# Kernel tuning notes

Measured on AMD Instinct MI355X. Metric: run time of the kernel, lower is better.

The kernel has to match this reference:

```python
import jax, jax.numpy as jnp
import numpy as np

DT = 0.02        # time step
DT_SKIP = DT * 20
ITERS = 49       # BDF2 iterations hardcoded in forward()
P = 64           # tronc (reduced dim)
NG_U = 8000      # HR sample count, u-equation
NG_V = 8000      # HR sample count, v-equation
B = 32           # batch of trajectories


def setup_inputs() -> dict:
    key = jax.random.key(0)
    k0, k1, k2, k3, k4 = jax.random.split(key, 5)
    state = jax.random.normal(k0, (B, P), dtype=jnp.float32)
    Ap = jax.random.normal(k1, (P, P), dtype=jnp.float32) * 0.05
    W_all_u = jax.random.normal(k2, (4 * NG_U, P), dtype=jnp.float32) * 0.02
    W_all_v = jax.random.normal(k3, (4 * NG_V, P), dtype=jnp.float32) * 0.02
    P_proj = jax.random.normal(k4, (P, NG_U + NG_V), dtype=jnp.float32) * 0.02
    return {"state": state, "Ap": Ap, "W_all_u": W_all_u,
            "W_all_v": W_all_v, "P_proj": P_proj}


def _rhs(a, W_all_u, W_all_v, P_proj):
    # a: (B, p) -> (B, p). Batched hyper-reduced quadratic RHS.
    zu = a @ W_all_u.T                       # (B, 4*Ng_u)
    uu, vu, dxu, dyu = jnp.split(zu, 4, axis=1)
    fu = uu * dxu + vu * dyu                 # (B, Ng_u)
    zv = a @ W_all_v.T                       # (B, 4*Ng_v)
    uv, vv, dxv, dyv = jnp.split(zv, 4, axis=1)
    fv = uv * dxv + vv * dyv                 # (B, Ng_v)
    concat = jnp.concatenate([fu, fv], axis=1)  # (B, Ng_u+Ng_v)
    return -(concat @ P_proj.T)              # (B, p)


def reference(state, Ap, W_all_u, W_all_v, P_proj):
    dt = jnp.float32(DT)
    a0 = state[:, :P]                        # state_rom (B, p)
    eye = jnp.eye(P, dtype=state.dtype)
    mat_1st = eye - dt * Ap[:P, :P]          # I - dt*A
    mat_2nd = 3.0 * eye - 2.0 * dt * Ap[:P, :P]

    # first step: implicit Euler
    f0 = _rhs(a0, W_all_u, W_all_v, P_proj)
    r0 = a0 + dt * f0
    a1 = jnp.linalg.solve(mat_1st, r0.T).T   # == lu_solve(LU_1st, ...)

    # BDF2 recurrence
    def step(carry, _):
        a_prev, f_prev, a_new = carry
        f_new = _rhs(a_new, W_all_u, W_all_v, P_proj)
        r = 4.0 * a_new - a_prev + 4.0 * dt * f_new - 2.0 * dt * f_prev
        a_next = jnp.linalg.solve(mat_2nd, r.T).T
        return (a_new, f_new, a_next), None

    (_, _, out_new), _ = jax.lax.scan(step, (a0, f0, a1), None, length=ITERS)
    return (out_new - a0) / jnp.float32(DT_SKIP)
```

## Files before the change

### kernel.cpp

```cpp
#include <hip/hip_runtime.h>

#define DTC 0.02f
#define INV_DT_SKIP 2.5f
#define NBLK 32
#define NSTEP 50

typedef __attribute__((ext_vector_type(8))) __bf16 bf16x8;
typedef __attribute__((ext_vector_type(4))) float f32x4;
typedef __attribute__((ext_vector_type(8))) unsigned short us8;
typedef unsigned long long u64t;

__device__ inline unsigned short f2bf(float x) {
    unsigned u = __float_as_uint(x);
    unsigned r = u + 0x7FFF + ((u >> 16) & 1u);
    return (unsigned short)(r >> 16);
}
__device__ inline float bf2f(unsigned short h) {
    return __uint_as_float(((unsigned)h) << 16);
}
__device__ inline unsigned short f2bf_force(float x, unsigned b) {
    unsigned u = __float_as_uint(x);
    unsigned short c1 = (unsigned short)(((u >> 16) & ~1u) | b);
    unsigned short c0 = (unsigned short)(c1 - 2);
    unsigned short c2 = (unsigned short)(c1 + 2);
    float d0 = fabsf(x - bf2f(c0));
    float d1 = fabsf(x - bf2f(c1));
    float d2 = fabsf(x - bf2f(c2));
    unsigned short h = c1; float d = d1;
    if (d0 < d) { h = c0; d = d0; }
    if (d2 < d) { h = c2; }
    return h;
}
__device__ inline void gstore32(unsigned* p, unsigned v) {
    __hip_atomic_store(p, v, __ATOMIC_RELAXED, __HIP_MEMORY_SCOPE_AGENT);
}
__device__ inline u64t gload64(const u64t* p) {
    return __hip_atomic_load(p, __ATOMIC_RELAXED, __HIP_MEMORY_SCOPE_AGENT);
}
#define PINV(x) asm volatile("" : "+v"(x))

__global__ __launch_bounds__(256) void kinv(const float* __restrict__ Ap,
                                            float* __restrict__ inv1,
                                            float* __restrict__ inv2,
                                            uint4* __restrict__ pz) {
    const int t = threadIdx.x;
    {
        const int gt = blockIdx.x * 256 + t;
        for (int i = gt; i < 16384; i += 512) pz[i] = (uint4){0u, 0u, 0u, 0u};
    }
    const float coef  = (blockIdx.x == 0) ? DTC : (2.0f * DTC / 3.0f);
    const float scale = (blockIdx.x == 0) ? 1.0f : (1.0f / 3.0f);
    float* outp = (blockIdx.x == 0) ? inv1 : inv2;

    __shared__ float ET[64 * 68];
    __shared__ float XA[64 * 68];
    __shared__ float XB[64 * 68];

    for (int idx = t; idx < 4096; idx += 256) {
        int r = idx >> 6, c = idx & 63;
        float e = coef * Ap[idx];
        ET[c * 68 + r] = e;
        XA[r * 68 + c] = ((r == c) ? 1.0f : 0.0f) + e;
    }
    __syncthreads();

    const int rr = (t >> 4) << 2;
    const int cc = (t & 15) << 2;
    float* bufs[2] = {XA, XB};
    for (int it = 0; it < 3; it++) {
        const float* Xin = bufs[it & 1];
        float* Xout = bufs[(it + 1) & 1];
        float acc[4][4];
        #pragma unroll
        for (int i = 0; i < 4; i++)
            #pragma unroll
            for (int j = 0; j < 4; j++)
                acc[i][j] = ((rr + i) == (cc + j)) ? 1.0f : 0.0f;
        for (int k = 0; k < 64; k++) {
            float4 e4 = *(const float4*)&ET[k * 68 + rr];
            float4 x4 = *(const float4*)&Xin[k * 68 + cc];
            float ev[4] = {e4.x, e4.y, e4.z, e4.w};
            float xv[4] = {x4.x, x4.y, x4.z, x4.w};
            #pragma unroll
            for (int i = 0; i < 4; i++)
                #pragma unroll
                for (int j = 0; j < 4; j++)
                    acc[i][j] += ev[i] * xv[j];
        }
        __syncthreads();
        #pragma unroll
        for (int i = 0; i < 4; i++)
            #pragma unroll
            for (int j = 0; j < 4; j++)
                Xout[(rr + i) * 68 + cc + j] = acc[i][j];
        __syncthreads();
    }
    const float* Xf = bufs[1];
    for (int idx = t; idx < 4096; idx += 256) {
        int r = idx >> 6, c = idx & 63;
        outp[idx] = scale * Xf[r * 68 + c];
    }
}

__global__ __launch_bounds__(512, 2)
void kmain(const float* __restrict__ state,
           const float* __restrict__ Wu,
           const float* __restrict__ Wv,
           const float* __restrict__ Pp,
           const float* __restrict__ inv1,
           const float* __restrict__ inv2,
           unsigned* __restrict__ pbuf,
           float* __restrict__ out) {
    const int t = threadIdx.x;
    const int l = t & 63;
    const int w = t >> 6;
    const int blk = blockIdx.x;
    const int gw = blk * 8 + w;
    const bool active = (gw < 250);

    __shared__ float Ab[3][2176];
    __shared__ float fb[8][16][36];
    __shared__ float red2[2][8][1056];
    __shared__ float rbuf[32 * 68];

    for (int i = t; i < 2048; i += 512) Ab[0][(i >> 6) * 68 + (i & 63)] = state[i];
    if (!active) {
        for (int i = l; i < 1056; i += 64) { red2[0][w][i] = 0.f; red2[1][w][i] = 0.f; }
    }

    const int nr = l & 15;
    const int c0 = (l >> 4) << 3;
    const int cA = gw * 2;
    const float* W = (cA < 250) ? Wu : Wv;
    const int glA = ((cA < 250) ? cA : cA - 250) * 32;

    bf16x8 wf[2][2][4][2], pf[2][4], sfw[2];
    if (active) {
        #pragma unroll
        for (int ch = 0; ch < 2; ch++)
            #pragma unroll
            for (int th = 0; th < 2; th++)
                #pragma unroll
                for (int rb = 0; rb < 4; rb++)
                    #pragma unroll
                    for (int kt = 0; kt < 2; kt++) {
                        const float* s = W + (size_t)(rb * 8000 + glA + ch * 32 + th * 16 + nr) * 64
                                           + kt * 32 + c0;
                        us8 o;
                        #pragma unroll
                        for (int j = 0; j < 8; j++) o[j] = f2bf(s[j]);
                        wf[ch][th][rb][kt] = __builtin_bit_cast(bf16x8, o);
                    }
        #pragma unroll
        for (int ch = 0; ch < 2; ch++)
            #pragma unroll
            for (int pt = 0; pt < 4; pt++) {
                const float* s = Pp + (size_t)(pt * 16 + nr) * 16000 + (cA + ch) * 32 + c0;
                us8 o;
                #pragma unroll
                for (int j = 0; j < 8; j++) o[j] = f2bf(s[j]);
                pf[ch][pt] = __builtin_bit_cast(bf16x8, o);
            }
    }
    {
        const int ptS = w & 3;
        #pragma unroll
        for (int kt = 0; kt < 2; kt++) {
            int p = ptS * 16 + nr;
            const float* s = inv2 + (size_t)p * 64 + kt * 32 + c0;
            us8 o;
            #pragma unroll
            for (int j = 0; j < 8; j++) {
                float v = s[j] - ((p == kt * 32 + c0 + j) ? (1.0f / 3.0f) : 0.0f);
                o[j] = f2bf(v);
            }
            sfw[kt] = __builtin_bit_cast(bf16x8, o);
        }
    }
    #pragma unroll
    for (int ch = 0; ch < 2; ch++) {
        #pragma unroll
        for (int th = 0; th < 2; th++)
            #pragma unroll
            for (int rb = 0; rb < 4; rb++)
                #pragma unroll
                for (int kt = 0; kt < 2; kt++) PINV(wf[ch][th][rb][kt]);
        #pragma unroll
        for (int pt = 0; pt < 4; pt++) PINV(pf[ch][pt]);
    }
    PINV(sfw[0]); PINV(sfw[1]);
    __syncthreads();

    int ia_prev = 2, ia_cur = 0, ia_next = 1;
    float fprev[4];

    for (int k = 0; k < NSTEP; k++) {
        const int par = k & 1;
        const unsigned tag2 = (unsigned)(k + 1) & 3u;
        unsigned* pslot = pbuf + (size_t)par * (NBLK * 1024) + blk * 1024;

        if (active) {
            const int col = l & 15, q4 = l >> 4;
            #pragma unroll
            for (int mt = 0; mt < 2; mt++) {
                bf16x8 ahi[2], alo[2];
                {
                    const float* ac = Ab[ia_cur];
                    #pragma unroll
                    for (int kt = 0; kt < 2; kt++) {
                        us8 hv, lv;
                        #pragma unroll
                        for (int j = 0; j < 8; j++) {
                            float x = ac[(mt * 16 + nr) * 68 + kt * 32 + c0 + j];
                            unsigned short h = f2bf(x);
                            hv[j] = h;
                            lv[j] = f2bf(x - bf2f(h));
                        }
                        ahi[kt] = __builtin_bit_cast(bf16x8, hv);
                        alo[kt] = __builtin_bit_cast(bf16x8, lv);
                    }
                }
                f32x4 racc[4] = {{0.f,0.f,0.f,0.f},{0.f,0.f,0.f,0.f},
                                 {0.f,0.f,0.f,0.f},{0.f,0.f,0.f,0.f}};
                #pragma unroll
                for (int ch = 0; ch < 2; ch++) {
                    #pragma unroll
                    for (int th = 0; th < 2; th++) {
                        f32x4 z[4];
                        #pragma unroll
                        for (int rb = 0; rb < 4; rb++) {
                            f32x4 acc = {0.f, 0.f, 0.f, 0.f};
                            #pragma unroll
                            for (int kt = 0; kt < 2; kt++) {
                                acc = __builtin_amdgcn_mfma_f32_16x16x32_bf16(ahi[kt], wf[ch][th][rb][kt], acc, 0, 0, 0);
                                acc = __builtin_amdgcn_mfma_f32_16x16x32_bf16(alo[kt], wf[ch][th][rb][kt], acc, 0, 0, 0);
                            }
                            z[rb] = acc;
                        }
                        #pragma unroll
                        for (int r = 0; r < 4; r++) {
                            float f = z[0][r] * z[2][r] + z[1][r] * z[3][r];
                            fb[w][q4 * 4 + r][th * 16 + col] = f;
                        }
                    }
                    bf16x8 ff;
                    {
                        us8 fv8;
                        #pragma unroll
                        for (int j = 0; j < 8; j++) fv8[j] = f2bf(fb[w][nr][c0 + j]);
                        ff = __builtin_bit_cast(bf16x8, fv8);
                    }
                    #pragma unroll
                    for (int pt = 0; pt < 4; pt++)
                        racc[pt] = __builtin_amdgcn_mfma_f32_16x16x32_bf16(ff, pf[ch][pt], racc[pt], 0, 0, 0);
                }
                #pragma unroll
                for (int pt = 0; pt < 4; pt++)
                    #pragma unroll
                    for (int r = 0; r < 4; r++)
                        red2[mt][w][q4 * 264 + r * 64 + pt * 16 + col] = racc[pt][r];
            }
        }
        __syncthreads();

        {
            const int q4e = t >> 7;
            const int rem = (2 * t) & 255;
            const int addr = q4e * 264 + rem;
            #pragma unroll
            for (int mt = 0; mt < 2; mt++) {
                float s0 = 0.f, s1 = 0.f;
                #pragma unroll
                for (int w8 = 0; w8 < 8; w8++) {
                    float2 p = *(const float2*)&red2[mt][w8][addr];
                    s0 += p.x;
                    s1 += p.y;
                }
                unsigned v = (unsigned)f2bf_force(s0, tag2 & 1u)
                           | ((unsigned)f2bf_force(s1, tag2 >> 1) << 16);
                gstore32(&pslot[mt * 512 + t], v);
            }
        }

        float rb_[4];
        const int bB = (4 * t) >> 6, p0B = (4 * t) & 63;
        {
            #pragma unroll
            for (int jj = 0; jj < 4; jj++) {
                int row = bB * 68 + p0B + jj;
                float av = Ab[ia_cur][row];
                rb_[jj] = (k == 0) ? av
                                   : (4.f * av - Ab[ia_prev][row] - 2.f * DTC * fprev[jj]);
            }
        }

        float fv[4];
        {
            const u64t* pb = (const u64t*)(pbuf + (size_t)par * (NBLK * 1024));
            const unsigned tagrep = (tag2 & 1u) | ((tag2 >> 1) << 16);
            float s0 = 0.f, s1 = 0.f, s2 = 0.f, s3 = 0.f;
            unsigned need = 0xFFFFFFFFu;
            for (;;) {
                u64t buf[NBLK];
                #pragma unroll
                for (int s = 0; s < NBLK; s++)
                    buf[s] = gload64(pb + (size_t)s * 512 + t);
                #pragma unroll
                for (int s = 0; s < NBLK; s++) {
                    unsigned lo = (unsigned)buf[s], hi = (unsigned)(buf[s] >> 32);
                    unsigned bad = ((lo ^ tagrep) | (hi ^ tagrep)) & 0x00010001u;
                    if (((need >> s) & 1u) && bad == 0u) {
                        s0 += __uint_as_float(lo << 16);
                        s1 += __uint_as_float(lo & 0xffff0000u);
                        s2 += __uint_as_float(hi << 16);
                        s3 += __uint_as_float(hi & 0xffff0000u);
                        need &= ~(1u << s);
                    }
                }
                if (!__any(need != 0u)) break;
                __builtin_amdgcn_s_sleep(2);
            }
            asm volatile("" ::: "memory");
            fv[0] = -s0; fv[1] = -s1; fv[2] = -s2; fv[3] = -s3;
        }

        {
            const float cf = (k == 0) ? DTC : 4.f * DTC;
            #pragma unroll
            for (int jj = 0; jj < 4; jj++) {
                float f = fv[jj];
                rbuf[bB * 68 + p0B + jj] = rb_[jj] + cf * f;
                fprev[jj] = f;
            }
        }
        __syncthreads();

        {
            const int mtS = w >> 2, ptS = w & 3;
            const int col = l & 15, q4 = l >> 4;
            bf16x8 S0, S1;
            float cb;
            if (k == 0) {
                #pragma unroll
                for (int kt = 0; kt < 2; kt++) {
                    int p = ptS * 16 + nr;
                    const float* s = inv1 + (size_t)p * 64 + kt * 32 + c0;
                    us8 o;
                    #pragma unroll
                    for (int j = 0; j < 8; j++) {
                        float v = s[j] - ((p == kt * 32 + c0 + j) ? 1.0f : 0.0f);
                        o[j] = f2bf(v);
                    }
                    if (kt == 0) S0 = __builtin_bit_cast(bf16x8, o);
                    else         S1 = __builtin_bit_cast(bf16x8, o);
                }
                cb = 1.0f;
            } else {
                S0 = sfw[0]; S1 = sfw[1];
                cb = 1.0f / 3.0f;
            }
            bf16x8 rhi[2], rlo[2];
            #pragma unroll
            for (int kt = 0; kt < 2; kt++) {
                us8 hv, lv;
                #pragma unroll
                for (int j = 0; j < 8; j++) {
                    float x = rbuf[(mtS * 16 + nr) * 68 + kt * 32 + c0 + j];
                    unsigned short h = f2bf(x);
                    hv[j] = h;
                    lv[j] = f2bf(x - bf2f(h));
                }
                rhi[kt] = __builtin_bit_cast(bf16x8, hv);
                rlo[kt] = __builtin_bit_cast(bf16x8, lv);
            }
            f32x4 acc;
            #pragma unroll
            for (int r = 0; r < 4; r++)
                acc[r] = rbuf[(mtS * 16 + q4 * 4 + r) * 68 + ptS * 16 + col] * cb;
            acc = __builtin_amdgcn_mfma_f32_16x16x32_bf16(rhi[0], S0, acc, 0, 0, 0);
            acc = __builtin_amdgcn_mfma_f32_16x16x32_bf16(rlo[0], S0, acc, 0, 0, 0);
            acc = __builtin_amdgcn_mfma_f32_16x16x32_bf16(rhi[1], S1, acc, 0, 0, 0);
            acc = __builtin_amdgcn_mfma_f32_16x16x32_bf16(rlo[1], S1, acc, 0, 0, 0);
            #pragma unroll
            for (int r = 0; r < 4; r++)
                Ab[ia_next][(mtS * 16 + q4 * 4 + r) * 68 + ptS * 16 + col] = acc[r];
        }
        __syncthreads();

        if (k == NSTEP - 1 && blk == 0) {
            for (int i = t; i < 2048; i += 512)
                out[i] = (Ab[ia_next][(i >> 6) * 68 + (i & 63)] - state[i]) * INV_DT_SKIP;
        }

        int tmp = ia_prev; ia_prev = ia_cur; ia_cur = ia_next; ia_next = tmp;
    }
}

extern "C" void kernel_launch(void* const* d_in, const int* in_sizes, int n_in,
                              void* d_out, int out_size, void* d_ws, size_t ws_size,
                              hipStream_t stream) {
    const float* state = (const float*)d_in[0];
    const float* Ap    = (const float*)d_in[1];
    const float* Wu    = (const float*)d_in[2];
    const float* Wv    = (const float*)d_in[3];
    const float* Pp    = (const float*)d_in[4];
    float* out = (float*)d_out;
    float* ws  = (float*)d_ws;

    float* inv1 = ws;
    float* inv2 = ws + 4096;
    unsigned* pbuf = (unsigned*)(ws + 8192);

    hipLaunchKernelGGL(kinv, dim3(2), dim3(256), 0, stream, Ap, inv1, inv2,
                       (uint4*)pbuf);
    hipLaunchKernelGGL(kmain, dim3(NBLK), dim3(512), 0, stream,
                       state, Wu, Wv, Pp, inv1, inv2, pbuf, out);
}
```

Measured before the change: 607.1 us.

## Add dedicated reducer block to aggregate cross-block partials and broadcast results

Adds an extra workgroup that polls all 32 blocks' tagged bf16 partial sums each step, reduces them once, and writes the fp32 result with a 2-bit tag into a small result buffer. The 32 worker blocks then poll only this compact buffer instead of each reading all 32 partial slots. This is meant to cut redundant global-memory polling traffic and per-block reduction work. In exchange it adds an extra hop of latency per step, and it steals the low two mantissa bits of each fp32 result to hold the tag.

Result: no change. 605.7 us (-0.2%).

```diff
diff --git a/kernel.cpp b/kernel.cpp
--- a/kernel.cpp
+++ b/kernel.cpp
@@ -34,6 +34,9 @@
 __device__ inline void gstore32(unsigned* p, unsigned v) {
     __hip_atomic_store(p, v, __ATOMIC_RELAXED, __HIP_MEMORY_SCOPE_AGENT);
 }
+__device__ inline void gstore64(u64t* p, u64t v) {
+    __hip_atomic_store(p, v, __ATOMIC_RELAXED, __HIP_MEMORY_SCOPE_AGENT);
+}
 __device__ inline u64t gload64(const u64t* p) {
     return __hip_atomic_load(p, __ATOMIC_RELAXED, __HIP_MEMORY_SCOPE_AGENT);
 }
@@ -46,7 +49,7 @@
     const int t = threadIdx.x;
     {
         const int gt = blockIdx.x * 256 + t;
-        for (int i = gt; i < 16384; i += 512) pz[i] = (uint4){0u, 0u, 0u, 0u};
+        for (int i = gt; i < 17408; i += 512) pz[i] = (uint4){0u, 0u, 0u, 0u};
     }
     const float coef  = (blockIdx.x == 0) ? DTC : (2.0f * DTC / 3.0f);
     const float scale = (blockIdx.x == 0) ? 1.0f : (1.0f / 3.0f);
@@ -110,11 +113,52 @@
            const float* __restrict__ inv1,
            const float* __restrict__ inv2,
            unsigned* __restrict__ pbuf,
+           unsigned* __restrict__ resbuf,
            float* __restrict__ out) {
     const int t = threadIdx.x;
     const int l = t & 63;
     const int w = t >> 6;
     const int blk = blockIdx.x;
+
+    if (blk == NBLK) {
+        for (int k = 0; k < NSTEP; k++) {
+            const int par = k & 1;
+            const unsigned tag2 = (unsigned)(k + 1) & 3u;
+            const unsigned tagrep = (tag2 & 1u) | ((tag2 >> 1) << 16);
+            const u64t* pb = (const u64t*)(pbuf + (size_t)par * (NBLK * 1024));
+            float s0 = 0.f, s1 = 0.f, s2 = 0.f, s3 = 0.f;
+            unsigned need = 0xFFFFFFFFu;
+            for (;;) {
+                u64t buf[NBLK];
+                #pragma unroll
+                for (int s = 0; s < NBLK; s++)
+                    buf[s] = gload64(pb + (size_t)s * 512 + t);
+                #pragma unroll
+                for (int s = 0; s < NBLK; s++) {
+                    unsigned lo = (unsigned)buf[s], hi = (unsigned)(buf[s] >> 32);
+                    unsigned bad = ((lo ^ tagrep) | (hi ^ tagrep)) & 0x00010001u;
+                    if (((need >> s) & 1u) && bad == 0u) {
+                        s0 += __uint_as_float(lo << 16);
+                        s1 += __uint_as_float(lo & 0xffff0000u);
+                        s2 += __uint_as_float(hi << 16);
+                        s3 += __uint_as_float(hi & 0xffff0000u);
+                        need &= ~(1u << s);
+                    }
+                }
+                if (!__any(need != 0u)) break;
+                __builtin_amdgcn_s_sleep(1);
+            }
+            unsigned* rw = resbuf + (size_t)par * 2048 + 4 * t;
+            unsigned q0 = (__float_as_uint(-s0) & ~3u) | tag2;
+            unsigned q1 = (__float_as_uint(-s1) & ~3u) | tag2;
+            unsigned q2 = (__float_as_uint(-s2) & ~3u) | tag2;
+            unsigned q3 = (__float_as_uint(-s3) & ~3u) | tag2;
+            gstore64((u64t*)rw,     (u64t)q0 | ((u64t)q1 << 32));
+            gstore64((u64t*)rw + 1, (u64t)q2 | ((u64t)q3 << 32));
+        }
+        return;
+    }
+
     const int gw = blk * 8 + w;
     const bool active = (gw < 250);
 
@@ -296,32 +340,23 @@
 
         float fv[4];
         {
-            const u64t* pb = (const u64t*)(pbuf + (size_t)par * (NBLK * 1024));
-            const unsigned tagrep = (tag2 & 1u) | ((tag2 >> 1) << 16);
-            float s0 = 0.f, s1 = 0.f, s2 = 0.f, s3 = 0.f;
-            unsigned need = 0xFFFFFFFFu;
+            const u64t* rp = (const u64t*)(resbuf + (size_t)par * 2048) + 2 * t;
             for (;;) {
-                u64t buf[NBLK];
-                #pragma unroll
-                for (int s = 0; s < NBLK; s++)
-                    buf[s] = gload64(pb + (size_t)s * 512 + t);
-                #pragma unroll
-                for (int s = 0; s < NBLK; s++) {
-                    unsigned lo = (unsigned)buf[s], hi = (unsigned)(buf[s] >> 32);
-                    unsigned bad = ((lo ^ tagrep) | (hi ^ tagrep)) & 0x00010001u;
-                    if (((need >> s) & 1u) && bad == 0u) {
-                        s0 += __uint_as_float(lo << 16);
-                        s1 += __uint_as_float(lo & 0xffff0000u);
-                        s2 += __uint_as_float(hi << 16);
-                        s3 += __uint_as_float(hi & 0xffff0000u);
-                        need &= ~(1u << s);
-                    }
-                }
-                if (!__any(need != 0u)) break;
-                __builtin_amdgcn_s_sleep(2);
+                u64t v0 = gload64(rp);
+                u64t v1 = gload64(rp + 1);
+                unsigned a0 = (unsigned)v0, a1 = (unsigned)(v0 >> 32);
+                unsigned d0 = (unsigned)v1, d1 = (unsigned)(v1 >> 32);
+                unsigned bad = ((a0 ^ tag2) | (a1 ^ tag2) | (d0 ^ tag2) | (d1 ^ tag2)) & 3u;
+                if (__all(bad == 0u)) {
+                    fv[0] = __uint_as_float(a0 & ~3u);
+                    fv[1] = __uint_as_float(a1 & ~3u);
+                    fv[2] = __uint_as_float(d0 & ~3u);
+                    fv[3] = __uint_as_float(d1 & ~3u);
+                    break;
+                }
+                __builtin_amdgcn_s_sleep(1);
             }
             asm volatile("" ::: "memory");
-            fv[0] = -s0; fv[1] = -s1; fv[2] = -s2; fv[3] = -s3;
         }
 
         {
@@ -409,10 +444,11 @@
 
     float* inv1 = ws;
     float* inv2 = ws + 4096;
-    unsigned* pbuf = (unsigned*)(ws + 8192);
+    unsigned* pbuf   = (unsigned*)(ws + 8192);
+    unsigned* resbuf = (unsigned*)(ws + 8192 + 65536);
 
     hipLaunchKernelGGL(kinv, dim3(2), dim3(256), 0, stream, Ap, inv1, inv2,
                        (uint4*)pbuf);
-    hipLaunchKernelGGL(kmain, dim3(NBLK), dim3(512), 0, stream,
-                       state, Wu, Wv, Pp, inv1, inv2, pbuf, out);
-}
+    hipLaunchKernelGGL(kmain, dim3(NBLK + 1), dim3(512), 0, stream,
+                       state, Wu, Wv, Pp, inv1, inv2, pbuf, resbuf, out);
+}
```
